# Performance work log

Measured on AMD Instinct MI355X. Metric: run time of the kernel, lower is better.

The kernel has to match this reference:

```python
import jax, jax.numpy as jnp
import numpy as np

TOL = 1e-3

def centered_grid(h, w):
    x = jnp.arange(w, dtype=jnp.float32) - (w - 1) / 2.0
    y = jnp.arange(h, dtype=jnp.float32) - (h - 1) / 2.0
    X = jnp.broadcast_to(x[None, :], (h, w))
    Y = jnp.broadcast_to(y[:, None], (h, w))
    return X, Y

def param_to_H(p):
    B = p.shape[0]
    z = jnp.zeros((B, 1, 1), dtype=p.dtype)
    return jnp.concatenate([p, z], axis=1).reshape(B, 3, 3) + jnp.eye(3, dtype=p.dtype)

def grid_sample_bilinear(A, xn, yn):
    # torch grid_sample, mode='bilinear', align_corners=False, padding_mode='zeros'
    B, k, h, w = A.shape
    ix = ((xn + 1.0) * w - 1.0) / 2.0
    iy = ((yn + 1.0) * h - 1.0) / 2.0
    x0 = jnp.floor(ix).astype(jnp.int32); x1 = x0 + 1
    y0 = jnp.floor(iy).astype(jnp.int32); y1 = y0 + 1
    wx1 = ix - x0.astype(ix.dtype); wx0 = 1.0 - wx1
    wy1 = iy - y0.astype(iy.dtype); wy0 = 1.0 - wy1
    def gather(xi, yi):
        valid = ((xi >= 0) & (xi <= w - 1) & (yi >= 0) & (yi <= h - 1)).astype(A.dtype)
        xc = jnp.clip(xi, 0, w - 1); yc = jnp.clip(yi, 0, h - 1)
        vals = jax.vmap(lambda a, yy, xx: a[:, yy, xx])(A, yc, xc)  # [B,k,h,w]
        return vals * valid[:, None, :, :]
    out = (gather(x0, y0) * (wx0 * wy0)[:, None]
           + gather(x1, y0) * (wx1 * wy0)[:, None]
           + gather(x0, y1) * (wx0 * wy1)[:, None]
           + gather(x1, y1) * (wx1 * wy1)[:, None])
    return out

def warp_hmg(img, p):
    B, k, h, w = img.shape
    X, Y = centered_grid(h, w)
    xy = jnp.stack([X.reshape(-1), Y.reshape(-1), jnp.ones(h * w, jnp.float32)], 0)  # [3,hw]
    H = param_to_H(p)
    xyw = jnp.einsum('bij,jn->bin', H, xy)
    Xw = (xyw[:, 0] / xyw[:, 2]).reshape(B, h, w) + (w - 1) / 2.0
    Yw = (xyw[:, 1] / xyw[:, 2]).reshape(B, h, w) + (h - 1) / 2.0
    xn = Xw / ((w - 1) / 2.0) - 1.0
    yn = Yw / ((h - 1) / 2.0) - 1.0
    Q = grid_sample_bilinear(img, xn, yn)
    mask = ((xn > -1 + 2.0 / w) & (xn < 1 - 2.0 / w)
            & (yn > -1 + 2.0 / h) & (yn < 1 - 2.0 / h)).astype(img.dtype)
    return Q, mask

def image_gradients(img):
    # central differences with replicate padding (matches GradientBatch)
    px = jnp.pad(img, ((0, 0), (0, 0), (0, 0), (1, 1)), mode='edge')
    dx = 0.5 * (px[..., 2:] - px[..., :-2])
    py = jnp.pad(img, ((0, 0), (0, 0), (1, 1), (0, 0)), mode='edge')
    dy = 0.5 * (py[..., 2:, :] - py[..., :-2, :])
    return dx, dy

def compute_dIdp(gx, gy):
    B, k, h, w = gx.shape
    X, Y = centered_grid(h, w)
    Xf = jnp.tile(X.reshape(-1), k)  # [k*h*w]
    Yf = jnp.tile(Y.reshape(-1), k)
    gx = gx.reshape(B, k * h * w)
    gy = gy.reshape(B, k * h * w)
    cols = [Xf * gx, Yf * gx, gx, Xf * gy, Yf * gy, gy,
            -Xf * Xf * gx - Xf * Yf * gy, -Xf * Yf * gx - Yf * Yf * gy]
    return jnp.stack(cols, axis=2)  # [B, k*h*w, 8]

def deeplk_forward(img, temp, max_itr):
    Fi, Ft = img, temp
    B, k, h, w = Ft.shape
    gx, gy = image_gradients(Ft)
    dIdp = compute_dIdp(gx, gy)                      # [B, N, 8]
    invH = jnp.linalg.inv(jnp.einsum('bni,bnj->bij', dIdp, dIdp))  # [B,8,8]
    invH_dIdp = jnp.einsum('bij,bnj->bin', invH, dIdp)             # [B,8,N]
    p0 = jnp.zeros((B, 8, 1), jnp.float32)
    dp0 = jnp.ones((B, 8, 1), jnp.float32)

    def step(carry, _):
        p, dp = carry
        Fi_warp, mask = warp_hmg(Fi, p)
        r = (Fi_warp - Ft * mask[:, None]).reshape(B, -1, 1)
        dp_new = jnp.einsum('bin,bnj->bij', invH_dIdp, r)
        dp_new = dp_new.at[:, 6:8, 0].set(0.0)
        cond = (jnp.linalg.norm(dp, axis=1, keepdims=True) > TOL).astype(p.dtype)
        dp2 = cond * dp_new  # per-sample gate: once converged dp stays 0 (matches torch while-loop)
        return (p - dp2, dp2), None

    (p, _), _ = jax.lax.scan(step, (p0, dp0), None, length=int(max_itr))
    return p, param_to_H(p)

def setup_inputs() -> dict:
    key = jax.random.key(0)
    k1, k2 = jax.random.split(key)
    img = jax.random.normal(k1, (16, 3, 256, 256), jnp.float32)
    temp = jax.random.normal(k2, (16, 3, 256, 256), jnp.float32)
    return {"img": img, "temp": temp, "max_itr": 20}

def reference(img, temp, max_itr):
    return deeplk_forward(img, temp, max_itr)
```

## Files before the change

### kernel.cpp

```cpp
#include <hip/hip_runtime.h>

#define BATCH 16
#define KCH 3
#define IH 256
#define IW 256
#define NPIX (IH*IW)
#define NITER 20
#define HCH 64
#define CH 16
#define SSLOTS 64
#define TPBF 256
#define TPBM 1024
#define NBLK (BATCH*CH)

#define AGENT __HIP_MEMORY_SCOPE_AGENT

struct Ws {
    float  hess_part[BATCH][HCH][36];
    double invH[BATCH][64];
    double s_part[2][BATCH][SSLOTS][8];
    double p[2][BATCH][8];
    double dpn2[2][BATCH];
    int    cnt[NITER][BATCH][32];
};

__device__ __forceinline__ double aload_d(const double* p) {
    return __hip_atomic_load(p, __ATOMIC_RELAXED, AGENT);
}
__device__ __forceinline__ void astore_d(double* p, double v) {
    __hip_atomic_store(p, v, __ATOMIC_RELAXED, AGENT);
}

__device__ __forceinline__ void pixel_accum(const float* __restrict__ I,
                                            const float* __restrict__ T,
                                            int x, int y,
                                            float h00, float h01, float h02,
                                            float h10, float h11, float h12,
                                            float* acc8, float* acc36, bool do_hess) {
    const float XL = -1.f + 2.f / IW, XH = 1.f - 2.f / IW;
    const float YL = -1.f + 2.f / IH, YH = 1.f - 2.f / IH;
    float X = (float)x - 127.5f, Y = (float)y - 127.5f;

    float Xw = (h00 * X + h01 * Y + h02) + 127.5f;
    float Yw = (h10 * X + h11 * Y + h12) + 127.5f;
    float xn = Xw / 127.5f - 1.f;
    float yn = Yw / 127.5f - 1.f;

    float ix = ((xn + 1.f) * (float)IW - 1.f) * 0.5f;
    float iy = ((yn + 1.f) * (float)IH - 1.f) * 0.5f;
    float fx0 = floorf(ix), fy0 = floorf(iy);
    int x0 = (int)fx0, y0 = (int)fy0;
    int x1 = x0 + 1, y1 = y0 + 1;
    float wx1 = ix - fx0, wx0 = 1.f - wx1;
    float wy1 = iy - fy0, wy0 = 1.f - wy1;

    bool vx0 = (x0 >= 0) && (x0 <= IW - 1), vx1 = (x1 >= 0) && (x1 <= IW - 1);
    bool vy0 = (y0 >= 0) && (y0 <= IH - 1), vy1 = (y1 >= 0) && (y1 <= IH - 1);
    int xc0 = min(max(x0, 0), IW - 1), xc1 = min(max(x1, 0), IW - 1);
    int yc0 = min(max(y0, 0), IH - 1), yc1 = min(max(y1, 0), IH - 1);

    float w00 = (wx0 * wy0) * ((vx0 && vy0) ? 1.f : 0.f);
    float w10 = (wx1 * wy0) * ((vx1 && vy0) ? 1.f : 0.f);
    float w01 = (wx0 * wy1) * ((vx0 && vy1) ? 1.f : 0.f);
    float w11 = (wx1 * wy1) * ((vx1 && vy1) ? 1.f : 0.f);

    float mask = (xn > XL && xn < XH && yn > YL && yn < YH) ? 1.f : 0.f;

#pragma unroll
    for (int c = 0; c < KCH; c++) {
        const float* Ic = I + c * NPIX;
        const float* Tc = T + c * NPIX;
        float v00 = Ic[yc0 * IW + xc0];
        float v10 = Ic[yc0 * IW + xc1];
        float v01 = Ic[yc1 * IW + xc0];
        float v11 = Ic[yc1 * IW + xc1];
        float Q = v00 * w00 + v10 * w10 + v01 * w01 + v11 * w11;
        float r = Q - Tc[y * IW + x] * mask;
        float gx = 0.5f * (Tc[y * IW + min(x + 1, IW - 1)] - Tc[y * IW + max(x - 1, 0)]);
        float gy = 0.5f * (Tc[min(y + 1, IH - 1) * IW + x] - Tc[max(y - 1, 0) * IW + x]);
        float gxr = gx * r, gyr = gy * r;
        float ur = X * gxr + Y * gyr;
        acc8[0] += X * gxr;
        acc8[1] += Y * gxr;
        acc8[2] += gxr;
        acc8[3] += X * gyr;
        acc8[4] += Y * gyr;
        acc8[5] += gyr;
        acc8[6] -= X * ur;
        acc8[7] -= Y * ur;
        if (do_hess) {
            float d[8];
            d[0] = X * gx; d[1] = Y * gx; d[2] = gx;
            d[3] = X * gy; d[4] = Y * gy; d[5] = gy;
            d[6] = -X * X * gx - X * Y * gy;
            d[7] = -X * Y * gx - Y * Y * gy;
            int idx = 0;
#pragma unroll
            for (int i = 0; i < 8; i++)
#pragma unroll
                for (int j = i; j < 8; j++) { acc36[idx] += d[i] * d[j]; idx++; }
        }
    }
}

__global__ __launch_bounds__(TPBF) void k_first(const float* __restrict__ img,
                                                const float* __restrict__ temp, Ws* ws) {
    const int b = blockIdx.y, chunk = blockIdx.x, t = threadIdx.x;
    const int lane = t & 63, wave = t >> 6;
    float acc8[8], acc36[36];
#pragma unroll
    for (int i = 0; i < 8; i++) acc8[i] = 0.f;
#pragma unroll
    for (int i = 0; i < 36; i++) acc36[i] = 0.f;
    const float* I = img + (size_t)b * KCH * NPIX;
    const float* T = temp + (size_t)b * KCH * NPIX;

#pragma unroll
    for (int pp = 0; pp < 4; ++pp)
        pixel_accum(I, T, t, chunk * 4 + pp, 1.f, 0.f, 0.f, 0.f, 1.f, 0.f,
                    acc8, acc36, true);

#pragma unroll
    for (int i = 0; i < 36; i++) {
        float v = acc36[i];
        for (int o = 32; o > 0; o >>= 1) v += __shfl_xor(v, o, 64);
        acc36[i] = v;
    }
#pragma unroll
    for (int i = 0; i < 8; i++) {
        float v = acc8[i];
        for (int o = 32; o > 0; o >>= 1) v += __shfl_xor(v, o, 64);
        acc8[i] = v;
    }
    __shared__ float red36[4][36];
    __shared__ float red8[4][8];
    if (lane == 0) {
#pragma unroll
        for (int i = 0; i < 36; i++) red36[wave][i] = acc36[i];
#pragma unroll
        for (int i = 0; i < 8; i++) red8[wave][i] = acc8[i];
    }
    __syncthreads();
    if (t < 36)
        ws->hess_part[b][chunk][t] = red36[0][t] + red36[1][t] + red36[2][t] + red36[3][t];
    if (t < 8)
        ws->s_part[0][b][chunk][t] =
            (double)(red8[0][t] + red8[1][t] + red8[2][t] + red8[3][t]);
}

__global__ __launch_bounds__(1024) void k_invert(Ws* ws) {
    const int t = threadIdx.x;
    {
        int* c = &ws->cnt[0][0][0];
        const int total = NITER * BATCH * 32;
        for (int i = t; i < total; i += 1024) c[i] = 0;
    }
    const int b = t >> 6, lane = t & 63;
    double hv = 0.0;
    if (lane < 36) {
        for (int c = 0; c < HCH; c++) hv += (double)ws->hess_part[b][c][lane];
    }
    const int ii = lane >> 3, jj = lane & 7;
    const int a = min(ii, jj), bb = max(ii, jj);
    const int pidx = a * 8 - a * (a - 1) / 2 + (bb - a);
    double Mv = __shfl(hv, pidx, 64);
    double Av = (ii == jj) ? 1.0 : 0.0;
#pragma unroll
    for (int k = 0; k < 8; k++) {
        double pivd = __shfl(Mv, k * 8 + k, 64);
        double inv = 1.0 / pivd;
        double rM = __shfl(Mv, k * 8 + jj, 64) * inv;
        double rA = __shfl(Av, k * 8 + jj, 64) * inv;
        double fac = __shfl(Mv, ii * 8 + k, 64);
        if (ii == k) { Mv = rM; Av = rA; }
        else         { Mv -= fac * rM; Av -= fac * rA; }
    }
    ws->invH[b][lane] = Av;
}

__device__ __forceinline__ void batchbar(Ws* ws, int it, int b) {
    asm volatile("s_waitcnt vmcnt(0)" ::: "memory");
    __syncthreads();
    if (threadIdx.x == 0) {
        __hip_atomic_fetch_add(&ws->cnt[it][b][0], 1, __ATOMIC_RELAXED, AGENT);
        while (__hip_atomic_load(&ws->cnt[it][b][0], __ATOMIC_RELAXED, AGENT) < CH)
            __builtin_amdgcn_s_sleep(8);
    }
    __syncthreads();
    asm volatile("" ::: "memory");
}

__global__ __launch_bounds__(TPBM) void mega_loop(const float* __restrict__ img,
                                                  const float* __restrict__ temp,
                                                  Ws* ws, float* __restrict__ out) {
    const int bid = blockIdx.x;
    const int b = bid & 15;
    const int chunk = bid >> 4;
    const int t = threadIdx.x;
    const int lane = t & 63, wave = t >> 6;
    const int x = t & 255, yrow = t >> 8;

    __shared__ double ir_sh[64];
    __shared__ float pf_sh[8];
    __shared__ float red8[16][8];

    const float* I = img + (size_t)b * KCH * NPIX;
    const float* T = temp + (size_t)b * KCH * NPIX;

    if (t < 64) ir_sh[t] = ws->invH[b][t];
    __syncthreads();

    double p_reg = 0.0, dpn2 = 8.0;
    for (int it = 1; it <= NITER; ++it) {
        if (wave == 0) {
            const int par = (it - 1) & 1;
            const int j = lane & 7, c_lo = lane >> 3;
            const int nm = (it == 1) ? 8 : 2;
            double sv = 0.0;
            for (int m = 0; m < nm; m++)
                sv += aload_d(&ws->s_part[par][b][c_lo + 8 * m][j]);
            sv += __shfl_xor(sv, 8, 64);
            sv += __shfl_xor(sv, 16, 64);
            sv += __shfl_xor(sv, 32, 64);
            double dp = 0.0;
#pragma unroll
            for (int jj = 0; jj < 8; jj++)
                dp += ir_sh[(lane & 7) * 8 + jj] * __shfl(sv, jj, 64);
            double d = (lane < 6 && dpn2 > 1e-6) ? dp : 0.0;
            double n2 = d * d;
            n2 += __shfl_xor(n2, 1, 64);
            n2 += __shfl_xor(n2, 2, 64);
            n2 += __shfl_xor(n2, 4, 64);
            p_reg -= d;
            dpn2 = n2;
            if (lane < 8) pf_sh[lane] = (float)p_reg;
        }
        __syncthreads();
        if (it == NITER) break;

        float pf[8];
#pragma unroll
        for (int jj = 0; jj < 8; jj++) pf[jj] = pf_sh[jj];

        float acc8[8];
#pragma unroll
        for (int i = 0; i < 8; i++) acc8[i] = 0.f;
#pragma unroll
        for (int pp = 0; pp < 4; ++pp)
            pixel_accum(I, T, x, chunk * 16 + yrow * 4 + pp,
                        1.f + pf[0], pf[1], pf[2], pf[3], 1.f + pf[4], pf[5],
                        acc8, nullptr, false);
#pragma unroll
        for (int i = 0; i < 8; i++) {
            float v = acc8[i];
            for (int o = 32; o > 0; o >>= 1) v += __shfl_xor(v, o, 64);
            acc8[i] = v;
        }
        if (lane == 0) {
#pragma unroll
            for (int i = 0; i < 8; i++) red8[wave][i] = acc8[i];
        }
        __syncthreads();
        if (t < 8) {
            float tot = 0.f;
#pragma unroll
            for (int w = 0; w < 16; w++) tot += red8[w][t];
            astore_d(&ws->s_part[it & 1][b][chunk][t], (double)tot);
        }
        batchbar(ws, it, b);
    }

    if (chunk == 0 && wave == 0) {
        if (lane < 8) {
            out[b * 8 + lane] = (float)p_reg;
            out[128 + b * 9 + lane] =
                (float)(p_reg + ((lane == 0 || lane == 4) ? 1.0 : 0.0));
        }
        if (lane == 8) out[128 + b * 9 + 8] = 1.0f;
    }
}

__device__ __forceinline__ double do_update_ws(const Ws* ws, int b, int it, int lane,
                                               double* n2_out) {
    const int par = (it - 1) & 1;
    const int j = lane & 7, c_lo = lane >> 3;
    double sv = 0.0;
#pragma unroll
    for (int m = 0; m < 8; m++) sv += ws->s_part[par][b][c_lo + 8 * m][j];
    sv += __shfl_xor(sv, 8, 64);
    sv += __shfl_xor(sv, 16, 64);
    sv += __shfl_xor(sv, 32, 64);
    const double* row = &ws->invH[b][(lane & 7) * 8];
    double dp = 0.0;
#pragma unroll
    for (int jj = 0; jj < 8; jj++) dp += row[jj] * __shfl(sv, jj, 64);
    double p_prev = 0.0, dpn2_prev = 8.0;
    if (it > 1) {
        if (lane < 8) p_prev = ws->p[par][b][lane];
        dpn2_prev = ws->dpn2[par][b];
    }
    double d = (lane < 6 && dpn2_prev > 1e-6) ? dp : 0.0;
    double n2 = d * d;
    n2 += __shfl_xor(n2, 1, 64);
    n2 += __shfl_xor(n2, 2, 64);
    n2 += __shfl_xor(n2, 4, 64);
    *n2_out = n2;
    return p_prev - d;
}

__global__ __launch_bounds__(TPBF) void k_iter(const float* __restrict__ img,
                                               const float* __restrict__ temp,
                                               Ws* ws, int it) {
    const int b = blockIdx.y, chunk = blockIdx.x, t = threadIdx.x;
    const int lane = t & 63, wave = t >> 6;
    double n2;
    double p_cur = do_update_ws(ws, b, it, lane, &n2);
    float pf[8];
#pragma unroll
    for (int jj = 0; jj < 8; jj++) pf[jj] = (float)__shfl(p_cur, jj, 64);
    if (chunk == 0 && wave == 0) {
        if (lane < 8) ws->p[it & 1][b][lane] = p_cur;
        if (lane == 0) ws->dpn2[it & 1][b] = n2;
    }
    float acc8[8];
#pragma unroll
    for (int i = 0; i < 8; i++) acc8[i] = 0.f;
    const float* I = img + (size_t)b * KCH * NPIX;
    const float* T = temp + (size_t)b * KCH * NPIX;
#pragma unroll
    for (int pp = 0; pp < 4; ++pp)
        pixel_accum(I, T, t, chunk * 4 + pp,
                    1.f + pf[0], pf[1], pf[2], pf[3], 1.f + pf[4], pf[5],
                    acc8, nullptr, false);
#pragma unroll
    for (int i = 0; i < 8; i++) {
        float v = acc8[i];
        for (int o = 32; o > 0; o >>= 1) v += __shfl_xor(v, o, 64);
        acc8[i] = v;
    }
    __shared__ float red8[4][8];
    if (lane == 0) {
#pragma unroll
        for (int i = 0; i < 8; i++) red8[wave][i] = acc8[i];
    }
    __syncthreads();
    if (t < 8)
        ws->s_part[it & 1][b][chunk][t] =
            (double)(red8[0][t] + red8[1][t] + red8[2][t] + red8[3][t]);
}

__global__ __launch_bounds__(1024) void k_out(Ws* ws, float* __restrict__ out) {
    const int t = threadIdx.x;
    const int b = t >> 6, lane = t & 63;
    double n2;
    double p_fin = do_update_ws(ws, b, NITER, lane, &n2);
    if (lane < 8) {
        out[b * 8 + lane] = (float)p_fin;
        out[128 + b * 9 + lane] =
            (float)(p_fin + ((lane == 0 || lane == 4) ? 1.0 : 0.0));
    }
    if (lane == 8) out[128 + b * 9 + 8] = 1.0f;
}

extern "C" void kernel_launch(void* const* d_in, const int* in_sizes, int n_in,
                              void* d_out, int out_size, void* d_ws, size_t ws_size,
                              hipStream_t stream) {
    const float* img  = (const float*)d_in[0];
    const float* temp = (const float*)d_in[1];
    Ws* ws = (Ws*)d_ws;
    float* out = (float*)d_out;

    k_first<<<dim3(HCH, BATCH), TPBF, 0, stream>>>(img, temp, ws);
    k_invert<<<1, 1024, 0, stream>>>(ws);

    int dev = 0, nCU = 0, maxB = 0;
    hipGetDevice(&dev);
    hipDeviceGetAttribute(&nCU, hipDeviceAttributeMultiprocessorCount, dev);
    hipError_t e = hipOccupancyMaxActiveBlocksPerMultiprocessor(
        &maxB, (const void*)mega_loop, TPBM, 0);
    const bool coop_ok = (e == hipSuccess) && ((long)maxB * nCU >= NBLK);

    if (coop_ok) {
        void* args[] = {(void*)&img, (void*)&temp, (void*)&ws, (void*)&out};
        hipLaunchCooperativeKernel((void*)mega_loop, dim3(NBLK), dim3(TPBM), args, 0,
                                   stream);
    } else {
        for (int it = 1; it < NITER; ++it)
            k_iter<<<dim3(HCH, BATCH), TPBF, 0, stream>>>(img, temp, ws, it);
        k_out<<<1, 1024, 0, stream>>>(ws, out);
    }
}
```

Measured before the change: 216.6 us.

## Cache template values and gradients in registers; compute params redundantly per wave

Template values and their central-difference gradients are now loaded once into registers before the iteration loop instead of being re-read every iteration inside pixel_accum. Every wave now redundantly reduces the partial sums and solves for dp, broadcasting p with shuffles, which removes a shared-memory round trip and a block barrier per iteration. The warp math is inlined with an affine-only projection. The barrier spin sleep is also shortened. The added register arrays raise register pressure at 1024 threads per block, and the redundant per-wave solve adds global loads.

```diff
diff --git a/kernel.cpp b/kernel.cpp
--- a/kernel.cpp
+++ b/kernel.cpp
@@ -184,7 +184,7 @@
     if (threadIdx.x == 0) {
         __hip_atomic_fetch_add(&ws->cnt[it][b][0], 1, __ATOMIC_RELAXED, AGENT);
         while (__hip_atomic_load(&ws->cnt[it][b][0], __ATOMIC_RELAXED, AGENT) < CH)
-            __builtin_amdgcn_s_sleep(8);
+            __builtin_amdgcn_s_sleep(4);
     }
     __syncthreads();
     asm volatile("" ::: "memory");
@@ -201,7 +201,6 @@
     const int x = t & 255, yrow = t >> 8;
 
     __shared__ double ir_sh[64];
-    __shared__ float pf_sh[8];
     __shared__ float red8[16][8];
 
     const float* I = img + (size_t)b * KCH * NPIX;
@@ -210,9 +209,28 @@
     if (t < 64) ir_sh[t] = ws->invH[b][t];
     __syncthreads();
 
+    float tcv[4][KCH], gxv[4][KCH], gyv[4][KCH];
+#pragma unroll
+    for (int pp = 0; pp < 4; ++pp) {
+        const int y = chunk * 16 + yrow * 4 + pp;
+        const int ym = max(y - 1, 0), yp = min(y + 1, IH - 1);
+        const int xm = max(x - 1, 0), xp = min(x + 1, IW - 1);
+#pragma unroll
+        for (int c = 0; c < KCH; c++) {
+            const float* Tc = T + c * NPIX;
+            tcv[pp][c] = Tc[y * IW + x];
+            gxv[pp][c] = 0.5f * (Tc[y * IW + xp] - Tc[y * IW + xm]);
+            gyv[pp][c] = 0.5f * (Tc[yp * IW + x] - Tc[ym * IW + x]);
+        }
+    }
+
+    const float XL = -1.f + 2.f / IW, XH = 1.f - 2.f / IW;
+    const float YL = -1.f + 2.f / IH, YH = 1.f - 2.f / IH;
+    const float Xc = (float)x - 127.5f;
+
     double p_reg = 0.0, dpn2 = 8.0;
     for (int it = 1; it <= NITER; ++it) {
-        if (wave == 0) {
+        {
             const int par = (it - 1) & 1;
             const int j = lane & 7, c_lo = lane >> 3;
             const int nm = (it == 1) ? 8 : 2;
@@ -233,23 +251,71 @@
             n2 += __shfl_xor(n2, 4, 64);
             p_reg -= d;
             dpn2 = n2;
-            if (lane < 8) pf_sh[lane] = (float)p_reg;
-        }
-        __syncthreads();
+        }
         if (it == NITER) break;
 
         float pf[8];
 #pragma unroll
-        for (int jj = 0; jj < 8; jj++) pf[jj] = pf_sh[jj];
+        for (int jj = 0; jj < 8; jj++) pf[jj] = (float)__shfl(p_reg, jj, 64);
+        const float h00 = 1.f + pf[0], h01 = pf[1], h02 = pf[2];
+        const float h10 = pf[3], h11 = 1.f + pf[4], h12 = pf[5];
 
         float acc8[8];
 #pragma unroll
         for (int i = 0; i < 8; i++) acc8[i] = 0.f;
-#pragma unroll
-        for (int pp = 0; pp < 4; ++pp)
-            pixel_accum(I, T, x, chunk * 16 + yrow * 4 + pp,
-                        1.f + pf[0], pf[1], pf[2], pf[3], 1.f + pf[4], pf[5],
-                        acc8, nullptr, false);
+
+#pragma unroll
+        for (int pp = 0; pp < 4; ++pp) {
+            const int y = chunk * 16 + yrow * 4 + pp;
+            const float Y = (float)y - 127.5f;
+
+            float Xw = (h00 * Xc + h01 * Y + h02) + 127.5f;
+            float Yw = (h10 * Xc + h11 * Y + h12) + 127.5f;
+            float xn = Xw / 127.5f - 1.f;
+            float yn = Yw / 127.5f - 1.f;
+
+            float ix = ((xn + 1.f) * (float)IW - 1.f) * 0.5f;
+            float iy = ((yn + 1.f) * (float)IH - 1.f) * 0.5f;
+            float fx0 = floorf(ix), fy0 = floorf(iy);
+            int x0 = (int)fx0, y0 = (int)fy0;
+            int x1 = x0 + 1, y1 = y0 + 1;
+            float wx1 = ix - fx0, wx0 = 1.f - wx1;
+            float wy1 = iy - fy0, wy0 = 1.f - wy1;
+
+            bool vx0 = (x0 >= 0) && (x0 <= IW - 1), vx1 = (x1 >= 0) && (x1 <= IW - 1);
+            bool vy0 = (y0 >= 0) && (y0 <= IH - 1), vy1 = (y1 >= 0) && (y1 <= IH - 1);
+            int xc0 = min(max(x0, 0), IW - 1), xc1 = min(max(x1, 0), IW - 1);
+            int yc0 = min(max(y0, 0), IH - 1), yc1 = min(max(y1, 0), IH - 1);
+
+            float w00 = (wx0 * wy0) * ((vx0 && vy0) ? 1.f : 0.f);
+            float w10 = (wx1 * wy0) * ((vx1 && vy0) ? 1.f : 0.f);
+            float w01 = (wx0 * wy1) * ((vx0 && vy1) ? 1.f : 0.f);
+            float w11 = (wx1 * wy1) * ((vx1 && vy1) ? 1.f : 0.f);
+
+            float mask = (xn > XL && xn < XH && yn > YL && yn < YH) ? 1.f : 0.f;
+
+#pragma unroll
+            for (int c = 0; c < KCH; c++) {
+                const float* Ic = I + c * NPIX;
+                float v00 = Ic[yc0 * IW + xc0];
+                float v10 = Ic[yc0 * IW + xc1];
+                float v01 = Ic[yc1 * IW + xc0];
+                float v11 = Ic[yc1 * IW + xc1];
+                float Q = v00 * w00 + v10 * w10 + v01 * w01 + v11 * w11;
+                float r = Q - tcv[pp][c] * mask;
+                float gxr = gxv[pp][c] * r, gyr = gyv[pp][c] * r;
+                float ur = Xc * gxr + Y * gyr;
+                acc8[0] += Xc * gxr;
+                acc8[1] += Y * gxr;
+                acc8[2] += gxr;
+                acc8[3] += Xc * gyr;
+                acc8[4] += Y * gyr;
+                acc8[5] += gyr;
+                acc8[6] -= Xc * ur;
+                acc8[7] -= Y * ur;
+            }
+        }
+
 #pragma unroll
         for (int i = 0; i < 8; i++) {
             float v = acc8[i];
```

Result: no change. 216.1 us (-0.2%).
